# Kernel tuning notes

Measured on AMD Instinct MI355X. Metric: run time of the kernel, lower is better.

## Reference

```python
import jax, jax.numpy as jnp
import numpy as np

B, C, H, W = 16, 384, 32, 32
K = 3  # depthwise kernel size


def setup_inputs() -> dict:
    key = jax.random.key(0)
    k1, k2, k3, k4, k5 = jax.random.split(key, 5)
    x = jax.random.normal(k1, (B, C, H, W), dtype=jnp.float32)
    # nn.Linear(C, 3C): weight [3C, C], bias [3C]
    lim = 1.0 / np.sqrt(C)
    w_qkv = jax.random.uniform(k2, (3 * C, C), minval=-lim, maxval=lim, dtype=jnp.float32)
    b_qkv = jax.random.uniform(k3, (3 * C,), minval=-lim, maxval=lim, dtype=jnp.float32)
    # depthwise Conv2d(C, C, K, padding=K//2, groups=C): weight [C, 1, K, K], bias [C]
    lim_c = 1.0 / np.sqrt(K * K)
    w_dw = jax.random.uniform(k4, (C, 1, K, K), minval=-lim_c, maxval=lim_c, dtype=jnp.float32)
    b_dw = jax.random.uniform(k5, (C,), minval=-lim_c, maxval=lim_c, dtype=jnp.float32)
    return {"x": x, "w_qkv": w_qkv, "b_qkv": b_qkv, "w_dw": w_dw, "b_dw": b_dw}


def _forward(x, w_qkv, b_qkv, w_dw, b_dw):
    Bx, Cx, Hx, Wx = x.shape
    N = Hx * Wx
    # x_flat: [B, N, C]
    x_flat = x.reshape(Bx, Cx, N).transpose(0, 2, 1)
    # qkv projection: [B, N, 3C] -> q, k, v each [B, N, C]
    qkv = jnp.einsum('bnc,oc->bno', x_flat, w_qkv) + b_qkv
    q, k, v = jnp.split(qkv, 3, axis=-1)
    # depthwise conv relative bias: [B, C, H, W] -> [B, N, C]
    rb = jax.lax.conv_general_dilated(
        x, w_dw, window_strides=(1, 1), padding='SAME',
        dimension_numbers=('NCHW', 'OIHW', 'NCHW'), feature_group_count=Cx)
    rb = rb + b_dw[None, :, None, None]
    rb = rb.reshape(Bx, Cx, N).transpose(0, 2, 1)
    # attention logits: q@k^T + q@rb^T == q @ (k + rb)^T  (no scaling in original)
    attn = jnp.einsum('bqc,bkc->bqk', q, k + rb)
    attn = jax.nn.softmax(attn, axis=-1)
    out_flat = jnp.einsum('bqk,bkc->bqc', attn, v)
    return out_flat.transpose(0, 2, 1).reshape(Bx, Cx, Hx, Wx)


def reference(x, w_qkv, b_qkv, w_dw, b_dw):
    return _forward(x, w_qkv, b_qkv, w_dw, b_dw)
```

## Files before the change

### kernel.cpp

```cpp
#include <hip/hip_runtime.h>

typedef _Float16 f16;
typedef _Float16 f16x8 __attribute__((ext_vector_type(8)));
typedef _Float16 f16x4 __attribute__((ext_vector_type(4)));
typedef float f32x4 __attribute__((ext_vector_type(4)));

#define LOG2E 1.44269504088896f

__global__ void k_wcvt(const float* __restrict__ w, f16* __restrict__ wh) {
    int i = (blockIdx.x * 256 + threadIdx.x) * 4;
    float4 v = *(const float4*)(w + i);
    f16x4 o = { (f16)v.x, (f16)v.y, (f16)v.z, (f16)v.w };
    *(f16x4*)(wh + i) = o;
}

__launch_bounds__(256)
__global__ void k_prep(const float* __restrict__ x, const float* __restrict__ wdw,
                       const float* __restrict__ bdw,
                       f16* __restrict__ xt, f16* __restrict__ rbt) {
    int ht = blockIdx.x, ct = blockIdx.y, b = blockIdx.z;
    __shared__ float xs[64 * 129];
    int t = threadIdx.x;
    int h0 = ht * 2;
#pragma unroll
    for (int i = 0; i < 8; ++i) {
        int idx = t + i * 256;
        int cl = idx >> 5, col4 = idx & 31;
        int hh = h0 - 1 + (col4 >> 3);
        int wq = (col4 & 7) * 4;
        float4 v = make_float4(0.f, 0.f, 0.f, 0.f);
        if (hh >= 0 && hh < 32)
            v = *(const float4*)(x + (size_t)(b * 384 + ct * 64 + cl) * 1024 + hh * 32 + wq);
        int base = cl * 129 + col4 * 4;
        xs[base] = v.x; xs[base + 1] = v.y; xs[base + 2] = v.z; xs[base + 3] = v.w;
    }
    __syncthreads();
    int cl = t & 63;
    int c = ct * 64 + cl;
    float wd[9];
#pragma unroll
    for (int k = 0; k < 9; ++k) wd[k] = wdw[c * 9 + k];
    float bd = bdw[c];
    const float* row = &xs[cl * 129];
    int nb = (t >> 6) * 16;
#pragma unroll
    for (int i = 0; i < 16; ++i) {
        int nl = nb + i;
        int hh = nl >> 5, ww = nl & 31;
        int lx = hh + 1;
        float acc = bd;
#pragma unroll
        for (int dh = -1; dh <= 1; ++dh) {
#pragma unroll
            for (int dw = -1; dw <= 1; ++dw) {
                int w2 = ww + dw;
                if (w2 >= 0 && w2 <= 31)
                    acc += wd[(dh + 1) * 3 + (dw + 1)] * row[(lx + dh) * 32 + w2];
            }
        }
        float xc = row[lx * 32 + ww];
        size_t at = ((size_t)(b * 1024) + h0 * 32 + nl) * 384 + c;
        rbt[at] = (f16)acc;
        xt[at] = (f16)xc;
    }
}

__launch_bounds__(256, 2)
__global__ void k_gemm1(const f16* __restrict__ xt, const f16* __restrict__ wh,
                        const float* __restrict__ bias, const f16* __restrict__ rbt,
                        f16* __restrict__ qo, f16* __restrict__ krb, f16* __restrict__ vt) {
    int bm = blockIdx.x, bn = blockIdx.y, b = blockIdx.z;
    __shared__ f16 As[128 * 64];
    __shared__ f16 Bs[128 * 64];
    int t = threadIdx.x;
    int lane = t & 63, wv = t >> 6;
    int wm = wv >> 1, wn = wv & 1;
    f32x4 acc[4][4] = {};
    const f16* xbase = xt + (size_t)(b * 1024 + bm * 128) * 384;
    const f16* wbase = wh + (size_t)(bn * 128) * 384;
    const bool vmode = (bn >= 6);
    for (int kc = 0; kc < 384; kc += 64) {
        __syncthreads();
#pragma unroll
        for (int i = 0; i < 4; ++i) {
            int idx = t + i * 256;
            int rowi = idx >> 3, x16 = idx & 7;
            int off = rowi * 128 + ((x16 * 16) ^ ((rowi & 7) << 4));
            uint4 da = *(const uint4*)(xbase + rowi * 384 + kc + x16 * 8);
            *(uint4*)((char*)As + off) = da;
            uint4 db = *(const uint4*)(wbase + rowi * 384 + kc + x16 * 8);
            *(uint4*)((char*)Bs + off) = db;
        }
        __syncthreads();
#pragma unroll
        for (int j = 0; j < 2; ++j) {
            f16x8 af[4], bf[4];
#pragma unroll
            for (int mr = 0; mr < 4; ++mr) {
                int rowi = wm * 64 + mr * 16 + (lane & 15);
                af[mr] = *(const f16x8*)((const char*)As + rowi * 128 +
                         ((j * 64 + (lane >> 4) * 16) ^ ((rowi & 7) << 4)));
            }
#pragma unroll
            for (int nr = 0; nr < 4; ++nr) {
                int rowi = wn * 64 + nr * 16 + (lane & 15);
                bf[nr] = *(const f16x8*)((const char*)Bs + rowi * 128 +
                         ((j * 64 + (lane >> 4) * 16) ^ ((rowi & 7) << 4)));
            }
            if (!vmode) {
#pragma unroll
                for (int mr = 0; mr < 4; ++mr)
#pragma unroll
                    for (int nr = 0; nr < 4; ++nr)
                        acc[mr][nr] = __builtin_amdgcn_mfma_f32_16x16x32_f16(af[mr], bf[nr], acc[mr][nr], 0, 0, 0);
            } else {
#pragma unroll
                for (int mr = 0; mr < 4; ++mr)
#pragma unroll
                    for (int nr = 0; nr < 4; ++nr)
                        acc[mr][nr] = __builtin_amdgcn_mfma_f32_16x16x32_f16(bf[nr], af[mr], acc[mr][nr], 0, 0, 0);
            }
        }
    }
    int o0 = bn * 128;
    if (!vmode) {
#pragma unroll
        for (int nr = 0; nr < 4; ++nr) {
            int o = o0 + wn * 64 + nr * 16 + (lane & 15);
            float bs = bias[o];
#pragma unroll
            for (int mr = 0; mr < 4; ++mr) {
                int n_l = wm * 64 + mr * 16 + ((lane >> 4) << 2);
#pragma unroll
                for (int r = 0; r < 4; ++r) {
                    int n_sp = bm * 128 + n_l + r;
                    size_t at = (size_t)(b * 1024 + n_sp) * 384;
                    float vv = acc[mr][nr][r] + bs;
                    if (o < 384) qo[at + o] = (f16)vv;
                    else krb[at + (o - 384)] = (f16)(vv + (float)rbt[at + (o - 384)]);
                }
            }
        }
    } else {
#pragma unroll
        for (int nr = 0; nr < 4; ++nr) {
#pragma unroll
            for (int mr = 0; mr < 4; ++mr) {
                int n_sp = bm * 128 + wm * 64 + mr * 16 + (lane & 15);
                int o_l = wn * 64 + nr * 16 + ((lane >> 4) << 2);
#pragma unroll
                for (int r = 0; r < 4; ++r) {
                    float vv = acc[mr][nr][r] + bias[o0 + o_l + r];
                    vt[(size_t)(b * 384 + (o0 - 768) + o_l + r) * 1024 + n_sp] = (f16)vv;
                }
            }
        }
    }
}

__launch_bounds__(256, 1)
__global__ void k_flash(const f16* __restrict__ q, const f16* __restrict__ krb,
                        const f16* __restrict__ vt, float* __restrict__ out) {
    int qt = blockIdx.x, b = blockIdx.y;
    __shared__ char smem[33792];
    f16* kvs = (f16*)smem;
    f16* ps  = (f16*)(smem + 16384);
    float* ot = (float*)smem;
    int t = threadIdx.x, lane = t & 63, wv = t >> 6;
    int n0 = qt * 64;
    f16x8 qf[12];
    {
        const f16* qb = q + (size_t)(b * 1024 + n0 + wv * 16 + (lane & 15)) * 384 + (lane >> 4) * 8;
#pragma unroll
        for (int ks = 0; ks < 12; ++ks) qf[ks] = *(const f16x8*)(qb + ks * 32);
    }
    f32x4 oa[24] = {};
    float m_run[4] = { -1e30f, -1e30f, -1e30f, -1e30f };
    float l_run[4] = { 0.f, 0.f, 0.f, 0.f };
    for (int kt = 0; kt < 16; ++kt) {
        f32x4 s[4] = {};
#pragma unroll
        for (int cc = 0; cc < 3; ++cc) {
            __syncthreads();
            const f16* kb = krb + (size_t)(b * 1024 + kt * 64) * 384 + cc * 128;
#pragma unroll
            for (int i = 0; i < 4; ++i) {
                int idx = t + i * 256;
                int rowi = idx >> 4, x16 = idx & 15;
                uint4 d = *(const uint4*)(kb + rowi * 384 + x16 * 8);
                *(uint4*)((char*)kvs + rowi * 256 + ((x16 * 16) ^ ((rowi & 7) << 4))) = d;
            }
            __syncthreads();
#pragma unroll
            for (int j = 0; j < 4; ++j) {
#pragma unroll
                for (int nr = 0; nr < 4; ++nr) {
                    int rowi = nr * 16 + (lane & 15);
                    f16x8 bf = *(const f16x8*)((const char*)kvs + rowi * 256 +
                               ((j * 64 + (lane >> 4) * 16) ^ ((rowi & 7) << 4)));
                    s[nr] = __builtin_amdgcn_mfma_f32_16x16x32_f16(qf[cc * 4 + j], bf, s[nr], 0, 0, 0);
                }
            }
        }
        float p[4][4];
#pragma unroll
        for (int r = 0; r < 4; ++r) {
            float m = fmaxf(fmaxf(s[0][r], s[1][r]), fmaxf(s[2][r], s[3][r]));
#pragma unroll
            for (int d = 1; d < 16; d <<= 1) m = fmaxf(m, __shfl_xor(m, d));
            float mn = fmaxf(m_run[r], m);
            float sc = exp2f((m_run[r] - mn) * LOG2E);
            m_run[r] = mn;
            float sum = 0.f;
#pragma unroll
            for (int nr = 0; nr < 4; ++nr) {
                float pv = exp2f((s[nr][r] - mn) * LOG2E);
                p[nr][r] = pv;
                sum += pv;
            }
#pragma unroll
            for (int d = 1; d < 16; d <<= 1) sum += __shfl_xor(sum, d);
            l_run[r] = l_run[r] * sc + sum;
#pragma unroll
            for (int cf = 0; cf < 24; ++cf) oa[cf][r] *= sc;
        }
#pragma unroll
        for (int nr = 0; nr < 4; ++nr)
#pragma unroll
            for (int r = 0; r < 4; ++r) {
                int prow = wv * 16 + ((lane >> 4) << 2) + r;
                int pcol = nr * 16 + (lane & 15);
                *(f16*)((char*)ps + prow * 128 + ((pcol * 2) ^ ((prow & 7) << 4))) = (f16)p[nr][r];
            }
        __syncthreads();
#pragma unroll
        for (int cc2 = 0; cc2 < 3; ++cc2) {
            const f16* vb = vt + (size_t)(b * 384 + cc2 * 128) * 1024 + kt * 64;
#pragma unroll
            for (int i = 0; i < 4; ++i) {
                int idx = t + i * 256;
                int rowi = idx >> 3, x16 = idx & 7;
                uint4 d = *(const uint4*)(vb + rowi * 1024 + x16 * 8);
                *(uint4*)((char*)kvs + rowi * 128 + ((x16 * 16) ^ ((rowi & 7) << 4))) = d;
            }
            __syncthreads();
#pragma unroll
            for (int j = 0; j < 2; ++j) {
                int prow = wv * 16 + (lane & 15);
                f16x8 pa = *(const f16x8*)((const char*)ps + prow * 128 +
                           ((j * 64 + (lane >> 4) * 16) ^ ((prow & 7) << 4)));
#pragma unroll
                for (int nr2 = 0; nr2 < 8; ++nr2) {
                    int rowi = nr2 * 16 + (lane & 15);
                    f16x8 bf = *(const f16x8*)((const char*)kvs + rowi * 128 +
                               ((j * 64 + (lane >> 4) * 16) ^ ((rowi & 7) << 4)));
                    oa[cc2 * 8 + nr2] = __builtin_amdgcn_mfma_f32_16x16x32_f16(pa, bf, oa[cc2 * 8 + nr2], 0, 0, 0);
                }
            }
            __syncthreads();
        }
    }
    float inv[4];
#pragma unroll
    for (int r = 0; r < 4; ++r) inv[r] = 1.0f / l_run[r];
#pragma unroll
    for (int cc2 = 0; cc2 < 3; ++cc2) {
        __syncthreads();
#pragma unroll
        for (int nr2 = 0; nr2 < 8; ++nr2) {
            int c_l = nr2 * 16 + (lane & 15);
            int qrow = wv * 16 + ((lane >> 4) << 2);
#pragma unroll
            for (int r = 0; r < 4; ++r)
                ot[c_l * 66 + qrow + r] = oa[cc2 * 8 + nr2][r] * inv[r];
        }
        __syncthreads();
        for (int rr = 0; rr < 32; ++rr) {
            int crow = wv * 32 + rr;
            out[(size_t)(b * 384 + cc2 * 128 + crow) * 1024 + n0 + lane] = ot[crow * 66 + lane];
        }
    }
}

extern "C" void kernel_launch(void* const* d_in, const int* in_sizes, int n_in,
                              void* d_out, int out_size, void* d_ws, size_t ws_size,
                              hipStream_t stream) {
    const float* x     = (const float*)d_in[0];
    const float* w_qkv = (const float*)d_in[1];
    const float* b_qkv = (const float*)d_in[2];
    const float* w_dw  = (const float*)d_in[3];
    const float* b_dw  = (const float*)d_in[4];
    float* out = (float*)d_out;
    char* ws = (char*)d_ws;
    const size_t SZ = (size_t)16 * 1024 * 384 * 2;
    f16* xt  = (f16*)(ws);
    f16* rbt = (f16*)(ws + SZ);
    f16* qo  = (f16*)(ws + 2 * SZ);
    f16* krb = (f16*)(ws + 3 * SZ);
    f16* vt  = (f16*)(ws + 4 * SZ);
    f16* wh  = (f16*)(ws + 5 * SZ);

    k_wcvt<<<432, 256, 0, stream>>>(w_qkv, wh);
    k_prep<<<dim3(16, 6, 16), 256, 0, stream>>>(x, w_dw, b_dw, xt, rbt);
    k_gemm1<<<dim3(8, 9, 16), 256, 0, stream>>>(xt, wh, b_qkv, rbt, qo, krb, vt);
    k_flash<<<dim3(16, 16), 256, 0, stream>>>(qo, krb, vt, out);
}
```

Baseline: 251.0 us.

## Restructure flash attention with transposed S, register P, and async LDS loads

The flash kernel now computes S^T (K as the A operand) over 32-key tiles and keeps the probabilities in registers, rebuilding the PV operand with lane shuffles instead of staging it through shared memory. It prefetches the next K tile and the current V tile with global_load_lds direct-to-LDS copies so they overlap the MFMA work. It also writes the output straight from registers without an LDS transpose, and raises wave priority around the MFMA blocks. The GEMM kernel likewise switches to global_load_lds staging with precomputed swizzled offsets. The trade-off is more loop iterations with smaller tiles, uncoalesced output stores, and a larger LDS footprint.

```diff
diff --git a/kernel.cpp b/kernel.cpp
--- a/kernel.cpp
+++ b/kernel.cpp
@@ -3,9 +3,16 @@
 typedef _Float16 f16;
 typedef _Float16 f16x8 __attribute__((ext_vector_type(8)));
 typedef _Float16 f16x4 __attribute__((ext_vector_type(4)));
+typedef _Float16 f16x2 __attribute__((ext_vector_type(2)));
 typedef float f32x4 __attribute__((ext_vector_type(4)));
 
-#define LOG2E 1.44269504088896f
+#define L2E 1.44269504088896f
+
+typedef __attribute__((address_space(1))) void GV;
+typedef __attribute__((address_space(3))) void LV;
+__device__ __forceinline__ void gl2lds(const void* gp, void* lp) {
+    __builtin_amdgcn_global_load_lds((GV*)gp, (LV*)lp, 16, 0, 0);
+}
 
 __global__ void k_wcvt(const float* __restrict__ w, f16* __restrict__ wh) {
     int i = (blockIdx.x * 256 + threadIdx.x) * 4;
@@ -69,27 +76,28 @@
 __global__ void k_gemm1(const f16* __restrict__ xt, const f16* __restrict__ wh,
                         const float* __restrict__ bias, const f16* __restrict__ rbt,
                         f16* __restrict__ qo, f16* __restrict__ krb, f16* __restrict__ vt) {
-    int bm = blockIdx.x, bn = blockIdx.y, b = blockIdx.z;
     __shared__ f16 As[128 * 64];
     __shared__ f16 Bs[128 * 64];
-    int t = threadIdx.x;
-    int lane = t & 63, wv = t >> 6;
+    int bm = blockIdx.x, bn = blockIdx.y, b = blockIdx.z;
+    int t = threadIdx.x, lane = t & 63, wv = t >> 6;
     int wm = wv >> 1, wn = wv & 1;
     f32x4 acc[4][4] = {};
-    const f16* xbase = xt + (size_t)(b * 1024 + bm * 128) * 384;
-    const f16* wbase = wh + (size_t)(bn * 128) * 384;
+    const char* xbase = (const char*)(xt + (size_t)(b * 1024 + bm * 128) * 384);
+    const char* wbase = (const char*)(wh + (size_t)(bn * 128) * 384);
     const bool vmode = (bn >= 6);
-    for (int kc = 0; kc < 384; kc += 64) {
+    int soff[4];
+#pragma unroll
+    for (int i = 0; i < 4; ++i) {
+        int idx = i * 256 + t;
+        int r = idx >> 3, cg = idx & 7;
+        soff[i] = r * 768 + ((cg ^ (r & 7)) << 4);
+    }
+    for (int kc = 0; kc < 6; ++kc) {
         __syncthreads();
 #pragma unroll
         for (int i = 0; i < 4; ++i) {
-            int idx = t + i * 256;
-            int rowi = idx >> 3, x16 = idx & 7;
-            int off = rowi * 128 + ((x16 * 16) ^ ((rowi & 7) << 4));
-            uint4 da = *(const uint4*)(xbase + rowi * 384 + kc + x16 * 8);
-            *(uint4*)((char*)As + off) = da;
-            uint4 db = *(const uint4*)(wbase + rowi * 384 + kc + x16 * 8);
-            *(uint4*)((char*)Bs + off) = db;
+            gl2lds(xbase + kc * 128 + soff[i], (char*)As + (i * 256 + wv * 64) * 16);
+            gl2lds(wbase + kc * 128 + soff[i], (char*)Bs + (i * 256 + wv * 64) * 16);
         }
         __syncthreads();
 #pragma unroll
@@ -107,6 +115,7 @@
                 bf[nr] = *(const f16x8*)((const char*)Bs + rowi * 128 +
                          ((j * 64 + (lane >> 4) * 16) ^ ((rowi & 7) << 4)));
             }
+            __builtin_amdgcn_s_setprio(1);
             if (!vmode) {
 #pragma unroll
                 for (int mr = 0; mr < 4; ++mr)
@@ -120,6 +129,7 @@
                     for (int nr = 0; nr < 4; ++nr)
                         acc[mr][nr] = __builtin_amdgcn_mfma_f32_16x16x32_f16(bf[nr], af[mr], acc[mr][nr], 0, 0, 0);
             }
+            __builtin_amdgcn_s_setprio(0);
         }
     }
     int o0 = bn * 128;
@@ -159,125 +169,143 @@
 }
 
 __launch_bounds__(256, 1)
-__global__ void k_flash(const f16* __restrict__ q, const f16* __restrict__ krb,
-                        const f16* __restrict__ vt, float* __restrict__ out) {
+__global__ void k_flash3(const f16* __restrict__ q, const f16* __restrict__ krb,
+                         const f16* __restrict__ vt, float* __restrict__ out) {
+    __shared__ char smem[49152];
+    char* Ks = smem;
+    char* Vs = smem + 24576;
     int qt = blockIdx.x, b = blockIdx.y;
-    __shared__ char smem[33792];
-    f16* kvs = (f16*)smem;
-    f16* ps  = (f16*)(smem + 16384);
-    float* ot = (float*)smem;
     int t = threadIdx.x, lane = t & 63, wv = t >> 6;
+    int g = lane >> 4, ln = lane & 15;
     int n0 = qt * 64;
+
     f16x8 qf[12];
     {
-        const f16* qb = q + (size_t)(b * 1024 + n0 + wv * 16 + (lane & 15)) * 384 + (lane >> 4) * 8;
-#pragma unroll
-        for (int ks = 0; ks < 12; ++ks) qf[ks] = *(const f16x8*)(qb + ks * 32);
-    }
-    f32x4 oa[24] = {};
-    float m_run[4] = { -1e30f, -1e30f, -1e30f, -1e30f };
-    float l_run[4] = { 0.f, 0.f, 0.f, 0.f };
-    for (int kt = 0; kt < 16; ++kt) {
-        f32x4 s[4] = {};
-#pragma unroll
-        for (int cc = 0; cc < 3; ++cc) {
-            __syncthreads();
-            const f16* kb = krb + (size_t)(b * 1024 + kt * 64) * 384 + cc * 128;
-#pragma unroll
-            for (int i = 0; i < 4; ++i) {
-                int idx = t + i * 256;
-                int rowi = idx >> 4, x16 = idx & 15;
-                uint4 d = *(const uint4*)(kb + rowi * 384 + x16 * 8);
-                *(uint4*)((char*)kvs + rowi * 256 + ((x16 * 16) ^ ((rowi & 7) << 4))) = d;
-            }
-            __syncthreads();
-#pragma unroll
-            for (int j = 0; j < 4; ++j) {
-#pragma unroll
-                for (int nr = 0; nr < 4; ++nr) {
-                    int rowi = nr * 16 + (lane & 15);
-                    f16x8 bf = *(const f16x8*)((const char*)kvs + rowi * 256 +
-                               ((j * 64 + (lane >> 4) * 16) ^ ((rowi & 7) << 4)));
-                    s[nr] = __builtin_amdgcn_mfma_f32_16x16x32_f16(qf[cc * 4 + j], bf, s[nr], 0, 0, 0);
-                }
-            }
-        }
-        float p[4][4];
+        const f16* qb = q + (size_t)(b * 1024 + n0 + wv * 16 + ln) * 384 + g * 8;
+#pragma unroll
+        for (int kc = 0; kc < 12; ++kc) qf[kc] = *(const f16x8*)(qb + kc * 32);
+    }
+
+    int koff[6], voff[6];
+#pragma unroll
+    for (int i = 0; i < 6; ++i) {
+        int idx = i * 256 + t;
+        int r = idx / 48, c = idx - r * 48;
+        koff[i] = r * 768 + ((c ^ (r & 7)) << 4);
+        int vr = idx >> 2, vc = idx & 3;
+        voff[i] = vr * 2048 + ((vc ^ (vr & 3)) << 4);
+    }
+    const char* kbase = (const char*)(krb + (size_t)b * 1024 * 384);
+    const char* vbase = (const char*)(vt + (size_t)b * 384 * 1024);
+
+#pragma unroll
+    for (int i = 0; i < 6; ++i)
+        gl2lds(kbase + koff[i], Ks + (i * 256 + wv * 64) * 16);
+
+    f32x4 oa[24];
+#pragma unroll
+    for (int i = 0; i < 24; ++i) oa[i] = (f32x4){0.f, 0.f, 0.f, 0.f};
+    float m_run = -1e30f, l_run = 0.f;
+    int src0 = 2 * (g & 1) * 16 + ln, src1 = src0 + 16;
+    bool gh = (g >= 2);
+
+    for (int kt = 0; kt < 32; ++kt) {
+        __syncthreads();
+#pragma unroll
+        for (int i = 0; i < 6; ++i)
+            gl2lds(vbase + kt * 64 + voff[i], Vs + (i * 256 + wv * 64) * 16);
+
+        f32x4 st[2] = {};
+        __builtin_amdgcn_s_setprio(1);
+#pragma unroll
+        for (int kc = 0; kc < 12; ++kc) {
+#pragma unroll
+            for (int nr = 0; nr < 2; ++nr) {
+                int kvr = nr * 16 + ln;
+                f16x8 kf = *(const f16x8*)(Ks + kvr * 768 +
+                            ((kc * 64 + g * 16) ^ ((kvr & 7) << 4)));
+                st[nr] = __builtin_amdgcn_mfma_f32_16x16x32_f16(kf, qf[kc], st[nr], 0, 0, 0);
+            }
+        }
+        __builtin_amdgcn_s_setprio(0);
+
+        float mx = st[0][0];
+#pragma unroll
+        for (int nr = 0; nr < 2; ++nr)
+#pragma unroll
+            for (int r = 0; r < 4; ++r) mx = fmaxf(mx, st[nr][r]);
+        mx = fmaxf(mx, __shfl_xor(mx, 16));
+        mx = fmaxf(mx, __shfl_xor(mx, 32));
+        float mn = fmaxf(m_run, mx);
+        float sc = exp2f((m_run - mn) * L2E);
+        m_run = mn;
+        float ls = 0.f;
+        float pv[2][4];
+#pragma unroll
+        for (int nr = 0; nr < 2; ++nr)
+#pragma unroll
+            for (int r = 0; r < 4; ++r) {
+                float p = exp2f((st[nr][r] - mn) * L2E);
+                pv[nr][r] = p;
+                ls += p;
+            }
+        ls += __shfl_xor(ls, 16);
+        ls += __shfl_xor(ls, 32);
+        l_run = l_run * sc + ls;
+#pragma unroll
+        for (int i = 0; i < 24; ++i) oa[i] *= sc;
+
+        int pk[4];
+#pragma unroll
+        for (int nr = 0; nr < 2; ++nr)
+#pragma unroll
+            for (int h = 0; h < 2; ++h) {
+                f16x2 w2 = { (f16)pv[nr][2 * h], (f16)pv[nr][2 * h + 1] };
+                pk[nr * 2 + h] = __builtin_bit_cast(int, w2);
+            }
+        f16x8 pb;
+        {
+            int a0 = __shfl(pk[0], src0);
+            int a1 = __shfl(pk[1], src0);
+            int a2 = __shfl(pk[2], src0);
+            int a3 = __shfl(pk[3], src0);
+            int b0 = __shfl(pk[0], src1);
+            int b1 = __shfl(pk[1], src1);
+            int b2 = __shfl(pk[2], src1);
+            int b3 = __shfl(pk[3], src1);
+            union { int w[4]; f16x8 v; } u;
+            u.w[0] = gh ? a2 : a0;
+            u.w[1] = gh ? a3 : a1;
+            u.w[2] = gh ? b2 : b0;
+            u.w[3] = gh ? b3 : b1;
+            pb = u.v;
+        }
+
+        __syncthreads();
+        if (kt < 31) {
+#pragma unroll
+            for (int i = 0; i < 6; ++i)
+                gl2lds(kbase + (kt + 1) * 24576 + koff[i], Ks + (i * 256 + wv * 64) * 16);
+        }
+
+        __builtin_amdgcn_s_setprio(1);
+#pragma unroll
+        for (int nr2 = 0; nr2 < 24; ++nr2) {
+            int cr = nr2 * 16 + ln;
+            f16x8 vf = *(const f16x8*)(Vs + cr * 64 +
+                        ((g * 16) ^ ((cr & 3) << 4)));
+            oa[nr2] = __builtin_amdgcn_mfma_f32_16x16x32_f16(vf, pb, oa[nr2], 0, 0, 0);
+        }
+        __builtin_amdgcn_s_setprio(0);
+    }
+
+    float inv = 1.0f / l_run;
+#pragma unroll
+    for (int nr2 = 0; nr2 < 24; ++nr2) {
 #pragma unroll
         for (int r = 0; r < 4; ++r) {
-            float m = fmaxf(fmaxf(s[0][r], s[1][r]), fmaxf(s[2][r], s[3][r]));
-#pragma unroll
-            for (int d = 1; d < 16; d <<= 1) m = fmaxf(m, __shfl_xor(m, d));
-            float mn = fmaxf(m_run[r], m);
-            float sc = exp2f((m_run[r] - mn) * LOG2E);
-            m_run[r] = mn;
-            float sum = 0.f;
-#pragma unroll
-            for (int nr = 0; nr < 4; ++nr) {
-                float pv = exp2f((s[nr][r] - mn) * LOG2E);
-                p[nr][r] = pv;
-                sum += pv;
-            }
-#pragma unroll
-            for (int d = 1; d < 16; d <<= 1) sum += __shfl_xor(sum, d);
-            l_run[r] = l_run[r] * sc + sum;
-#pragma unroll
-            for (int cf = 0; cf < 24; ++cf) oa[cf][r] *= sc;
-        }
-#pragma unroll
-        for (int nr = 0; nr < 4; ++nr)
-#pragma unroll
-            for (int r = 0; r < 4; ++r) {
-                int prow = wv * 16 + ((lane >> 4) << 2) + r;
-                int pcol = nr * 16 + (lane & 15);
-                *(f16*)((char*)ps + prow * 128 + ((pcol * 2) ^ ((prow & 7) << 4))) = (f16)p[nr][r];
-            }
-        __syncthreads();
-#pragma unroll
-        for (int cc2 = 0; cc2 < 3; ++cc2) {
-            const f16* vb = vt + (size_t)(b * 384 + cc2 * 128) * 1024 + kt * 64;
-#pragma unroll
-            for (int i = 0; i < 4; ++i) {
-                int idx = t + i * 256;
-                int rowi = idx >> 3, x16 = idx & 7;
-                uint4 d = *(const uint4*)(vb + rowi * 1024 + x16 * 8);
-                *(uint4*)((char*)kvs + rowi * 128 + ((x16 * 16) ^ ((rowi & 7) << 4))) = d;
-            }
-            __syncthreads();
-#pragma unroll
-            for (int j = 0; j < 2; ++j) {
-                int prow = wv * 16 + (lane & 15);
-                f16x8 pa = *(const f16x8*)((const char*)ps + prow * 128 +
-                           ((j * 64 + (lane >> 4) * 16) ^ ((prow & 7) << 4)));
-#pragma unroll
-                for (int nr2 = 0; nr2 < 8; ++nr2) {
-                    int rowi = nr2 * 16 + (lane & 15);
-                    f16x8 bf = *(const f16x8*)((const char*)kvs + rowi * 128 +
-                               ((j * 64 + (lane >> 4) * 16) ^ ((rowi & 7) << 4)));
-                    oa[cc2 * 8 + nr2] = __builtin_amdgcn_mfma_f32_16x16x32_f16(pa, bf, oa[cc2 * 8 + nr2], 0, 0, 0);
-                }
-            }
-            __syncthreads();
-        }
-    }
-    float inv[4];
-#pragma unroll
-    for (int r = 0; r < 4; ++r) inv[r] = 1.0f / l_run[r];
-#pragma unroll
-    for (int cc2 = 0; cc2 < 3; ++cc2) {
-        __syncthreads();
-#pragma unroll
-        for (int nr2 = 0; nr2 < 8; ++nr2) {
-            int c_l = nr2 * 16 + (lane & 15);
-            int qrow = wv * 16 + ((lane >> 4) << 2);
-#pragma unroll
-            for (int r = 0; r < 4; ++r)
-                ot[c_l * 66 + qrow + r] = oa[cc2 * 8 + nr2][r] * inv[r];
-        }
-        __syncthreads();
-        for (int rr = 0; rr < 32; ++rr) {
-            int crow = wv * 32 + rr;
-            out[(size_t)(b * 384 + cc2 * 128 + crow) * 1024 + n0 + lane] = ot[crow * 66 + lane];
+            int c = nr2 * 16 + g * 4 + r;
+            out[(size_t)(b * 384 + c) * 1024 + n0 + wv * 16 + ln] = oa[nr2][r] * inv;
         }
     }
 }
@@ -303,5 +331,5 @@
     k_wcvt<<<432, 256, 0, stream>>>(w_qkv, wh);
     k_prep<<<dim3(16, 6, 16), 256, 0, stream>>>(x, w_dw, b_dw, xt, rbt);
     k_gemm1<<<dim3(8, 9, 16), 256, 0, stream>>>(xt, wh, b_qkv, rbt, qo, krb, vt);
-    k_flash<<<dim3(16, 16), 256, 0, stream>>>(qo, krb, vt, out);
-}
+    k_flash3<<<dim3(16, 16), 256, 0, stream>>>(qo, krb, vt, out);
+}
```

Result: faster. 207.1 us (-17.5%).
